# Optimization experiments

Hardware: AMD Instinct MI355X
Metric: run time of the kernel (lower is better)

## Reference

```python
import jax, jax.numpy as jnp
import numpy as np

B, F, ND, NE = 1024, 1024, 256, 256

def setup_inputs() -> dict:
    key = jax.random.key(0)
    k1, k2, k3 = jax.random.split(key, 3)
    x = jax.random.normal(k1, (B, F), dtype=jnp.float32)
    # xavier-uniform-like init scale for (F+1, units)
    lim_d = float(np.sqrt(6.0 / (F + 1 + ND)))
    lim_e = float(np.sqrt(6.0 / (F + 1 + NE)))
    dilations = jax.random.uniform(k2, (F + 1, ND), minval=-lim_d, maxval=lim_d, dtype=jnp.float32)
    erosions = jax.random.uniform(k3, (F + 1, NE), minval=-lim_e, maxval=lim_e, dtype=jnp.float32)
    return {"x": x, "dilations": dilations, "erosions": erosions}

def reference(x, dilations, erosions):
    b = x.shape[0]
    # append a zero 'bias' feature -> (b, F+1)
    xb = jnp.concatenate([x, jnp.zeros((b, 1), dtype=x.dtype)], axis=1)
    # tropical matmuls: max-plus (dilation), min-minus (erosion)
    dilated = jnp.max(xb[:, :, None] + dilations[None, :, :], axis=1)   # (b, ND)
    eroded = jnp.min(xb[:, :, None] - erosions[None, :, :], axis=1)     # (b, NE)
    return jnp.concatenate([eroded, dilated], axis=1)
```

## Files before the change

### kernel.cpp

```cpp
#include <hip/hip_runtime.h>
#include <math.h>

#define BB   1024
#define FF   1024
#define NOUT 512
#define NW   256
#define BT   128
#define NT   64
#define KT   32

template<bool ERO>
__device__ __forceinline__ void core(
    float (* __restrict__ lds_x)[BT],
    float (* __restrict__ lds_w)[NT],
    const float* __restrict__ x,
    const float* __restrict__ w,
    float* __restrict__ dst,
    const int c0w, const int ks, const int ch)
{
    const int tid = threadIdx.x;
    const int cg  = tid & 7;
    const int rg  = tid >> 3;
    const int r0  = blockIdx.y * BT;
    const int bz  = blockIdx.z;

    float acc[4][8];
#pragma unroll
    for (int i = 0; i < 4; ++i)
#pragma unroll
        for (int j = 0; j < 8; ++j) acc[i][j] = -INFINITY;

    const int fstart = bz * ch;
    const int nchunk = ch / KT;

    for (int kc = 0; kc < nchunk; ++kc) {
        const int fb = fstart + kc * KT;
        if (kc) __syncthreads();

#pragma unroll
        for (int it = 0; it < 4; ++it) {
            const int tt = tid + it * 256;
            const int r = tt & 127;
            const int g = tt >> 7;
            const float4 v = *(const float4*)(x + (size_t)(r0 + r) * FF + fb + g * 4);
            lds_x[g * 4 + 0][r] = v.x;
            lds_x[g * 4 + 1][r] = v.y;
            lds_x[g * 4 + 2][r] = v.z;
            lds_x[g * 4 + 3][r] = v.w;
        }
#pragma unroll
        for (int it = 0; it < 2; ++it) {
            const int tt = tid + it * 256;
            const int f = tt >> 4;
            const int c4 = tt & 15;
            *(float4*)&lds_w[f][c4 * 4] =
                *(const float4*)(w + (size_t)(fb + f) * NW + c0w + c4 * 4);
        }
        __syncthreads();

#pragma unroll
        for (int ff = 0; ff < KT; ff += 2) {
            const float4 x0  = *(const float4*)&lds_x[ff][rg << 2];
            const float4 x1  = *(const float4*)&lds_x[ff + 1][rg << 2];
            const float4 wa0 = *(const float4*)&lds_w[ff][cg << 3];
            const float4 wb0 = *(const float4*)&lds_w[ff][(cg << 3) + 4];
            const float4 wa1 = *(const float4*)&lds_w[ff + 1][cg << 3];
            const float4 wb1 = *(const float4*)&lds_w[ff + 1][(cg << 3) + 4];
            const float xr0[4] = {x0.x, x0.y, x0.z, x0.w};
            const float xr1[4] = {x1.x, x1.y, x1.z, x1.w};
            const float wc0[8] = {wa0.x, wa0.y, wa0.z, wa0.w, wb0.x, wb0.y, wb0.z, wb0.w};
            const float wc1[8] = {wa1.x, wa1.y, wa1.z, wa1.w, wb1.x, wb1.y, wb1.z, wb1.w};
#pragma unroll
            for (int i = 0; i < 4; ++i)
#pragma unroll
                for (int j = 0; j < 8; ++j) {
                    const float t0 = ERO ? (wc0[j] - xr0[i]) : (xr0[i] + wc0[j]);
                    const float t1 = ERO ? (wc1[j] - xr1[i]) : (xr1[i] + wc1[j]);
                    acc[i][j] = fmaxf(acc[i][j], fmaxf(t0, t1));
                }
        }
    }

    if (bz == ks - 1) {
        const float4 ba = *(const float4*)(w + (size_t)FF * NW + c0w + (cg << 3));
        const float4 bb = *(const float4*)(w + (size_t)FF * NW + c0w + (cg << 3) + 4);
        const float bc[8] = {ba.x, ba.y, ba.z, ba.w, bb.x, bb.y, bb.z, bb.w};
#pragma unroll
        for (int i = 0; i < 4; ++i)
#pragma unroll
            for (int j = 0; j < 8; ++j) acc[i][j] = fmaxf(acc[i][j], bc[j]);
    }

    const int cglob = blockIdx.x * NT + (cg << 3);
#pragma unroll
    for (int i = 0; i < 4; ++i) {
        const int row = r0 + (rg << 2) + i;
        float4 v0, v1;
        v0.x = ERO ? -acc[i][0] : acc[i][0];
        v0.y = ERO ? -acc[i][1] : acc[i][1];
        v0.z = ERO ? -acc[i][2] : acc[i][2];
        v0.w = ERO ? -acc[i][3] : acc[i][3];
        v1.x = ERO ? -acc[i][4] : acc[i][4];
        v1.y = ERO ? -acc[i][5] : acc[i][5];
        v1.z = ERO ? -acc[i][6] : acc[i][6];
        v1.w = ERO ? -acc[i][7] : acc[i][7];
        *(float4*)(dst + (size_t)row * NOUT + cglob)     = v0;
        *(float4*)(dst + (size_t)row * NOUT + cglob + 4) = v1;
    }
}

__global__ __launch_bounds__(256, 2) void trop_main(
    const float* __restrict__ x,
    const float* __restrict__ dil,
    const float* __restrict__ ero,
    float* __restrict__ dst,
    const int ks, const int ch, const int direct)
{
    __shared__ float lds_x[KT][BT];
    __shared__ float lds_w[KT][NT];
    float* base = direct ? dst : dst + (size_t)blockIdx.z * (BB * NOUT);
    const int bx = blockIdx.x;
    if (bx < NW / NT) {
        core<true >(lds_x, lds_w, x, ero, base, bx * NT,      ks, ch);
    } else {
        core<false>(lds_x, lds_w, x, dil, base, bx * NT - NW, ks, ch);
    }
}

__global__ __launch_bounds__(256) void trop_combine(
    const float* __restrict__ ws, float* __restrict__ out, int ks)
{
    const int i4 = blockIdx.x * blockDim.x + threadIdx.x;
    const int col4 = (i4 << 2) & (NOUT - 1);
    const bool ero = col4 < NW;
    const int stride4 = BB * NOUT / 4;
    float4 v = ((const float4*)ws)[i4];
    for (int z = 1; z < ks; ++z) {
        const float4 u = ((const float4*)ws)[(size_t)z * stride4 + i4];
        if (ero) {
            v.x = fminf(v.x, u.x); v.y = fminf(v.y, u.y);
            v.z = fminf(v.z, u.z); v.w = fminf(v.w, u.w);
        } else {
            v.x = fmaxf(v.x, u.x); v.y = fmaxf(v.y, u.y);
            v.z = fmaxf(v.z, u.z); v.w = fmaxf(v.w, u.w);
        }
    }
    ((float4*)out)[i4] = v;
}

extern "C" void kernel_launch(void* const* d_in, const int* in_sizes, int n_in,
                              void* d_out, int out_size, void* d_ws, size_t ws_size,
                              hipStream_t stream) {
    const float* x   = (const float*)d_in[0];
    const float* dil = (const float*)d_in[1];
    const float* ero = (const float*)d_in[2];
    float* out = (float*)d_out;

    const size_t outbytes = (size_t)BB * NOUT * sizeof(float);
    int ks = 1;
    if      (ws_size >= 16 * outbytes) ks = 16;
    else if (ws_size >=  8 * outbytes) ks = 8;
    else if (ws_size >=  4 * outbytes) ks = 4;
    else if (ws_size >=  2 * outbytes) ks = 2;

    if (ks > 1) {
        dim3 grid(NOUT / NT, BB / BT, ks);
        trop_main<<<grid, 256, 0, stream>>>(x, dil, ero, (float*)d_ws, ks, FF / ks, 0);
        const int n4 = BB * NOUT / 4;
        trop_combine<<<n4 / 256, 256, 0, stream>>>((const float*)d_ws, out, ks);
    } else {
        dim3 grid(NOUT / NT, BB / BT, 1);
        trop_main<<<grid, 256, 0, stream>>>(x, dil, ero, out, 1, FF, 1);
    }
}
```

Measured before the change: 94.75 us.

## Always split-K into 16 partials using a static device buffer

Replaces the workspace-size-dependent split-K choice with a fixed 16-way split over the feature dimension. Partial results go to a statically allocated global array instead of the caller's workspace. With a small workspace the old code could fall back to very few blocks, so this guarantees enough parallelism to fill the GPU. The combine kernel now issues all 16 partial loads up front for more memory-level parallelism. The cost is a fixed 32 MB device buffer plus extra write and read traffic for the partials.

```diff
diff --git a/kernel.cpp b/kernel.cpp
--- a/kernel.cpp
+++ b/kernel.cpp
@@ -8,6 +8,9 @@
 #define BT   128
 #define NT   64
 #define KT   32
+#define KS   16
+
+__device__ float g_part[KS][BB * NOUT];
 
 template<bool ERO>
 __device__ __forceinline__ void core(
@@ -15,8 +18,7 @@
     float (* __restrict__ lds_w)[NT],
     const float* __restrict__ x,
     const float* __restrict__ w,
-    float* __restrict__ dst,
-    const int c0w, const int ks, const int ch)
+    const int c0w, const int ch)
 {
     const int tid = threadIdx.x;
     const int cg  = tid & 7;
@@ -81,7 +83,7 @@
         }
     }
 
-    if (bz == ks - 1) {
+    if (bz == KS - 1) {
         const float4 ba = *(const float4*)(w + (size_t)FF * NW + c0w + (cg << 3));
         const float4 bb = *(const float4*)(w + (size_t)FF * NW + c0w + (cg << 3) + 4);
         const float bc[8] = {ba.x, ba.y, ba.z, ba.w, bb.x, bb.y, bb.z, bb.w};
@@ -91,6 +93,7 @@
             for (int j = 0; j < 8; ++j) acc[i][j] = fmaxf(acc[i][j], bc[j]);
     }
 
+    float* dst = g_part[bz];
     const int cglob = blockIdx.x * NT + (cg << 3);
 #pragma unroll
     for (int i = 0; i < 4; ++i) {
@@ -113,36 +116,38 @@
     const float* __restrict__ x,
     const float* __restrict__ dil,
     const float* __restrict__ ero,
-    float* __restrict__ dst,
-    const int ks, const int ch, const int direct)
+    const int ch)
 {
     __shared__ float lds_x[KT][BT];
     __shared__ float lds_w[KT][NT];
-    float* base = direct ? dst : dst + (size_t)blockIdx.z * (BB * NOUT);
     const int bx = blockIdx.x;
     if (bx < NW / NT) {
-        core<true >(lds_x, lds_w, x, ero, base, bx * NT,      ks, ch);
+        core<true >(lds_x, lds_w, x, ero, bx * NT,      ch);
     } else {
-        core<false>(lds_x, lds_w, x, dil, base, bx * NT - NW, ks, ch);
+        core<false>(lds_x, lds_w, x, dil, bx * NT - NW, ch);
     }
 }
 
-__global__ __launch_bounds__(256) void trop_combine(
-    const float* __restrict__ ws, float* __restrict__ out, int ks)
+__global__ __launch_bounds__(256) void trop_combine(float* __restrict__ out)
 {
     const int i4 = blockIdx.x * blockDim.x + threadIdx.x;
     const int col4 = (i4 << 2) & (NOUT - 1);
     const bool ero = col4 < NW;
-    const int stride4 = BB * NOUT / 4;
-    float4 v = ((const float4*)ws)[i4];
-    for (int z = 1; z < ks; ++z) {
-        const float4 u = ((const float4*)ws)[(size_t)z * stride4 + i4];
+
+    float4 u[KS];
+#pragma unroll
+    for (int z = 0; z < KS; ++z)
+        u[z] = ((const float4*)g_part[z])[i4];
+
+    float4 v = u[0];
+#pragma unroll
+    for (int z = 1; z < KS; ++z) {
         if (ero) {
-            v.x = fminf(v.x, u.x); v.y = fminf(v.y, u.y);
-            v.z = fminf(v.z, u.z); v.w = fminf(v.w, u.w);
+            v.x = fminf(v.x, u[z].x); v.y = fminf(v.y, u[z].y);
+            v.z = fminf(v.z, u[z].z); v.w = fminf(v.w, u[z].w);
         } else {
-            v.x = fmaxf(v.x, u.x); v.y = fmaxf(v.y, u.y);
-            v.z = fmaxf(v.z, u.z); v.w = fmaxf(v.w, u.w);
+            v.x = fmaxf(v.x, u[z].x); v.y = fmaxf(v.y, u[z].y);
+            v.z = fmaxf(v.z, u[z].z); v.w = fmaxf(v.w, u[z].w);
         }
     }
     ((float4*)out)[i4] = v;
@@ -155,21 +160,10 @@
     const float* dil = (const float*)d_in[1];
     const float* ero = (const float*)d_in[2];
     float* out = (float*)d_out;
+    (void)d_ws; (void)ws_size;
 
-    const size_t outbytes = (size_t)BB * NOUT * sizeof(float);
-    int ks = 1;
-    if      (ws_size >= 16 * outbytes) ks = 16;
-    else if (ws_size >=  8 * outbytes) ks = 8;
-    else if (ws_size >=  4 * outbytes) ks = 4;
-    else if (ws_size >=  2 * outbytes) ks = 2;
-
-    if (ks > 1) {
-        dim3 grid(NOUT / NT, BB / BT, ks);
-        trop_main<<<grid, 256, 0, stream>>>(x, dil, ero, (float*)d_ws, ks, FF / ks, 0);
-        const int n4 = BB * NOUT / 4;
-        trop_combine<<<n4 / 256, 256, 0, stream>>>((const float*)d_ws, out, ks);
-    } else {
-        dim3 grid(NOUT / NT, BB / BT, 1);
-        trop_main<<<grid, 256, 0, stream>>>(x, dil, ero, out, 1, FF, 1);
-    }
+    dim3 grid(NOUT / NT, BB / BT, KS);
+    trop_main<<<grid, 256, 0, stream>>>(x, dil, ero, FF / KS);
+    const int n4 = BB * NOUT / 4;
+    trop_combine<<<n4 / 256, 256, 0, stream>>>(out);
 }
```

Result: no change. 96.17 us (+1.5%).
